# Kernel optimization log

Hardware: AMD Instinct MI355X
Metric: run time of the kernel (lower is better)

Reference implementation:

```python
import jax, jax.numpy as jnp
import numpy as np

H, W, R = 512, 512, 4
H8, W8 = H // 8, W // 8  # 64, 64
B, C = 4, 256


def _offsets(r):
    # diamond window: y in [-r, r], x in [|y|-r, r-|y|]  ->  2r^2+2r+1 offsets
    offs = []
    for y in range(-r, r + 1):
        for x in range(abs(y) - r, r - abs(y) + 1):
            offs.append((y, x))
    return np.asarray(offs, dtype=np.float32)  # [L, 2] = (dy, dx)

_OFFS = _offsets(R)  # L = 41


def _corr_pyramid(f1, f2):
    # over the second image's spatial dims for each pyramid level.
    c = jnp.einsum('bcij,bcuv->bijuv', f1, f2) / jnp.sqrt(jnp.float32(f1.shape[1]))
    pyr = [c]
    for _ in range(3):
        b, i, j, h, w = pyr[-1].shape
        pyr.append(pyr[-1].reshape(b, i, j, h // 2, 2, w // 2, 2).mean(axis=(4, 6)))
    return pyr  # shapes [B,64,64,64/2^k,64/2^k] for k=0..3


def _bilinear_zeros(volf, py, px, h, w):
    # volf: [B,H8,W8,h*w]; py/px: [B,H8,W8,L] pixel coords; zero padding.
    y0 = jnp.floor(py); x0 = jnp.floor(px)
    wy1 = py - y0; wy0 = 1.0 - wy1
    wx1 = px - x0; wx0 = 1.0 - wx1

    def gather(yi, xi):
        valid = (yi >= 0) & (yi < h) & (xi >= 0) & (xi < w)
        yc = jnp.clip(yi, 0, h - 1).astype(jnp.int32)
        xc = jnp.clip(xi, 0, w - 1).astype(jnp.int32)
        v = jnp.take_along_axis(volf, yc * w + xc, axis=-1)
        return jnp.where(valid, v, jnp.zeros((), volf.dtype))

    return (wy0 * wx0 * gather(y0, x0) + wy0 * wx1 * gather(y0, x0 + 1)
            + wy1 * wx0 * gather(y0 + 1, x0) + wy1 * wx1 * gather(y0 + 1, x0 + 1))


def _lookup_level(corr, flow, k):
    # corr: [B,H8,W8,h,w]; flow: [B,2,H8,W8] (chan 0 = dy, chan 1 = dx)
    b, _, _, h, w = corr.shape
    dy = jnp.asarray(_OFFS[:, 0]); dx = jnp.asarray(_OFFS[:, 1])
    ii = jnp.arange(H8, dtype=corr.dtype)[:, None]   # [H8,1]
    jj = jnp.arange(W8, dtype=corr.dtype)[None, :]   # [1,W8]
    scale = jnp.float32(2.0 ** k)
    yc = (ii[None] + flow[:, 0]) / scale             # [B,H8,W8]
    xc = (jj[None] + flow[:, 1]) / scale
    py = yc[..., None] + dy                          # [B,H8,W8,L]
    px = xc[..., None] + dx
    # original normalizes by dim/2 (not (dim-1)/2), grid_sample align_corners=True
    # maps normalized g -> pixel (g+1)*(dim-1)/2, net: pixel = coord*(dim-1)/dim
    py = py * (h - 1) / h
    px = px * (w - 1) / w
    volf = corr.reshape(b, H8, W8, h * w)
    return _bilinear_zeros(volf, py, px, h, w)       # [B,H8,W8,L]


def setup_inputs() -> dict:
    key = jax.random.key(0)
    k1, k2, k3 = jax.random.split(key, 3)
    feat1 = jax.random.normal(k1, (B, C, H8, W8), dtype=jnp.float32)
    feat2 = jax.random.normal(k2, (B, C, H8, W8), dtype=jnp.float32)
    curr_flow = jax.random.normal(k3, (B, 2, H8, W8), dtype=jnp.float32)
    return {"feat1": feat1, "feat2": feat2, "curr_flow": curr_flow}


def reference(feat1, feat2, curr_flow):
    pyr = _corr_pyramid(feat1, feat2)
    lookups = [_lookup_level(pyr[k], curr_flow, k) for k in range(4)]
    return jnp.stack(lookups, axis=3)  # [B, H8, W8, 4, 41]
```

## Files before the change

kernel.cpp:

```cpp
#include <hip/hip_runtime.h>
#include <stdint.h>

#define NB 4
#define NC 256
#define FB   1392640
#define LVO1 1048576
#define LVO2 1310720
#define LVO3 1376256

typedef short bf16x8 __attribute__((ext_vector_type(8)));
typedef float f32x4  __attribute__((ext_vector_type(4)));

__device__ __forceinline__ unsigned short f2b(float x){
  uint32_t u = __float_as_uint(x);
  return (unsigned short)((u + 0x7FFFu + ((u >> 16) & 1u)) >> 16);
}
__device__ __forceinline__ unsigned int pack2(float a, float b){
  return (unsigned int)f2b(a) | ((unsigned int)f2b(b) << 16);
}

__global__ __launch_bounds__(256) void prep_all(const float* __restrict__ f2,
                 unsigned short* __restrict__ f2c){
  __shared__ float lds[128*65];
  __shared__ float l1s[32*65];
  __shared__ float l2s[8*65];
  const int t = threadIdx.x;
  const int fid = blockIdx.x;
  const int b = fid >> 7, rest = fid & 127;
  const int reg = rest >> 2, cc = rest & 3;
  const int i0 = (reg >> 2) * 8, j0 = (reg & 3) * 16;
  const int c0 = cc * 64, qb = cc * 8;

  #pragma unroll
  for (int it = 0; it < 8; ++it){
    int q = t + 256*it;
    int ch = q >> 5, rc = q & 31, ri = rc >> 2, c4 = rc & 3;
    const float4 v = *(const float4*)(f2 + ((size_t)(b*NC) + c0 + ch)*4096
                                        + (i0+ri)*64 + j0 + c4*4);
    float* dstL = lds + (ri*16 + c4*4)*65 + ch;
    dstL[0] = v.x; dstL[65] = v.y; dstL[130] = v.z; dstL[195] = v.w;
  }
  __syncthreads();
  unsigned short* f2cB = f2c + (size_t)b*FB;

  #pragma unroll
  for (int it = 0; it < 4; ++it){
    int idx = t + 256*it;
    int cell = idx & 127, qi = idx >> 7;
    int ci = cell >> 4, cj = cell & 15;
    const float* src = lds + cell*65 + qi*8;
    uint4 v;
    v.x = pack2(src[0], src[1]); v.y = pack2(src[2], src[3]);
    v.z = pack2(src[4], src[5]); v.w = pack2(src[6], src[7]);
    int cellg = (i0+ci)*64 + j0+cj;
    *(uint4*)(f2cB + ((size_t)(qb+qi)*4096 + cellg)*8) = v;
  }
  {
    int cell = t & 31, qi = t >> 5;
    int a = cell >> 3, bc = cell & 7;
    const float* p00 = lds + ((2*a)*16 + 2*bc)*65 + qi*8;
    float s[8];
    #pragma unroll
    for (int j = 0; j < 8; ++j){
      s[j] = p00[j] + p00[65+j] + p00[16*65+j] + p00[17*65+j];
      l1s[cell*65 + qi*8 + j] = s[j];
    }
    uint4 v;
    v.x = pack2(s[0]*0.25f, s[1]*0.25f); v.y = pack2(s[2]*0.25f, s[3]*0.25f);
    v.z = pack2(s[4]*0.25f, s[5]*0.25f); v.w = pack2(s[6]*0.25f, s[7]*0.25f);
    int cellg = ((i0>>1)+a)*32 + (j0>>1)+bc;
    *(uint4*)(f2cB + LVO1 + ((size_t)(qb+qi)*1024 + cellg)*8) = v;
  }
  __syncthreads();
  if (t < 64){
    int cell = t & 7, qi = t >> 3;
    int a2 = cell >> 2, bc2 = cell & 3;
    float s[8];
    #pragma unroll
    for (int j = 0; j < 8; ++j){
      int ch = qi*8 + j;
      s[j] = l1s[((2*a2)*8   + 2*bc2  )*65 + ch] + l1s[((2*a2)*8   + 2*bc2+1)*65 + ch]
           + l1s[((2*a2+1)*8 + 2*bc2  )*65 + ch] + l1s[((2*a2+1)*8 + 2*bc2+1)*65 + ch];
      l2s[cell*65 + ch] = s[j];
    }
    uint4 v;
    v.x = pack2(s[0]*0.0625f, s[1]*0.0625f); v.y = pack2(s[2]*0.0625f, s[3]*0.0625f);
    v.z = pack2(s[4]*0.0625f, s[5]*0.0625f); v.w = pack2(s[6]*0.0625f, s[7]*0.0625f);
    int cellg = ((i0>>2)+a2)*16 + (j0>>2)+bc2;
    *(uint4*)(f2cB + LVO2 + ((size_t)(qb+qi)*256 + cellg)*8) = v;
  }
  __syncthreads();
  if (t < 16){
    int cl = t & 1, qi = t >> 1;
    float s[8];
    #pragma unroll
    for (int j = 0; j < 8; ++j){
      int ch = qi*8 + j;
      s[j] = l2s[(0*4 + 2*cl)*65 + ch] + l2s[(0*4 + 2*cl+1)*65 + ch]
           + l2s[(1*4 + 2*cl)*65 + ch] + l2s[(1*4 + 2*cl+1)*65 + ch];
    }
    const float m = 1.0f/64.0f;
    uint4 v;
    v.x = pack2(s[0]*m, s[1]*m); v.y = pack2(s[2]*m, s[3]*m);
    v.z = pack2(s[4]*m, s[5]*m); v.w = pack2(s[6]*m, s[7]*m);
    int cellg = (i0>>3)*8 + (j0>>3) + cl;
    *(uint4*)(f2cB + LVO3 + ((size_t)(qb+qi)*64 + cellg)*8) = v;
  }
}

__global__ __launch_bounds__(256, 4) void lookup_main(const float* __restrict__ flow,
                 const float* __restrict__ f1,
                 const unsigned short* __restrict__ f2c,
                 float* __restrict__ out){
  const int lane = threadIdx.x & 63;
  const int wid  = threadIdx.x >> 6;
  const int blk = blockIdx.x;
  const int xs = blk & 7;
  const int bb = xs >> 1;
  const int tile = ((blk >> 3) << 1) | (xs & 1);
  const int ti4 = (tile >> 4) << 2;
  const int tj4 = (tile & 15) << 2;

  __shared__ float box[4*16*113];
  __shared__ unsigned short f1s[16*264];
  __shared__ int   ls_y0[64], ls_x0[64];
  __shared__ float ls_f[32];
  __shared__ int   ls_meta[32];

  {
    float4* b4 = (float4*)box;
    for (int q = threadIdx.x; q < (4*16*113)/4; q += 256)
      b4[q] = make_float4(0.f, 0.f, 0.f, 0.f);
  }

  {
    const float* f1b = f1 + ((size_t)(bb*NC) + threadIdx.x)*4096;
    #pragma unroll
    for (int r = 0; r < 4; ++r){
      const float4 v = *(const float4*)(f1b + (ti4 + r)*64 + tj4);
      const int px = r*4;
      f1s[(px+0)*264 + threadIdx.x] = f2b(v.x);
      f1s[(px+1)*264 + threadIdx.x] = f2b(v.y);
      f1s[(px+2)*264 + threadIdx.x] = f2b(v.z);
      f1s[(px+3)*264 + threadIdx.x] = f2b(v.w);
    }
  }

  const int n = lane & 15;
  const int g = lane >> 4;
  const int pn = ((ti4 + (n >> 2)) << 6) + tj4 + (n & 3);

  if (wid == 0){
    const int k = g;
    const int i_n = pn >> 6, j_n = pn & 63;
    const float fy = flow[((bb*2 + 0)*64 + i_n)*64 + j_n];
    const float fx = flow[((bb*2 + 1)*64 + i_n)*64 + j_n];
    if (k == 0){ ls_f[n] = fy; ls_f[16 + n] = fx; }
    const int h = 64 >> k;
    const float inv = 1.0f / (float)(1 << k);
    const float s = (float)(h - 1) / (float)h;
    const float yc = ((float)i_n + fy) * inv;
    const float xc = ((float)j_n + fx) * inv;
    const int y0 = (int)floorf((yc - 4.0f) * s);
    const int x0 = (int)floorf((xc - 4.0f) * s);
    ls_y0[k*16 + n] = y0;
    ls_x0[k*16 + n] = x0;
    int ymin = y0, ymax = y0, xmin = x0, xmax = x0;
    #pragma unroll
    for (int m = 1; m < 16; m <<= 1){
      ymin = min(ymin, __shfl_xor(ymin, m));
      ymax = max(ymax, __shfl_xor(ymax, m));
      xmin = min(xmin, __shfl_xor(xmin, m));
      xmax = max(xmax, __shfl_xor(xmax, m));
    }
    if (n == 0){
      int ylo = max(ymin, 0), yhi = min(ymax + 9, h - 1);
      int xlo = max(xmin, 0), xhi = min(xmax + 9, h - 1);
      int H = max(yhi - ylo + 1, 0), W = max(xhi - xlo + 1, 0);
      int cells = W * H;
      ls_meta[k*8 + 0] = ylo;
      ls_meta[k*8 + 1] = xlo;
      ls_meta[k*8 + 2] = W;
      ls_meta[k*8 + 3] = cells;
      ls_meta[k*8 + 4] = __float_as_int(1.0f / (float)W);
      ls_meta[k*8 + 5] = (k==0) ? 0 : (k==1) ? LVO1 : (k==2) ? LVO2 : LVO3;
      ls_meta[k*8 + 6] = (cells + 15) >> 4;
    }
  }
  __syncthreads();

  bf16x8 bfr[8];
  #pragma unroll
  for (int st = 0; st < 8; ++st)
    bfr[st] = *(const bf16x8*)(&f1s[n*264 + st*32 + g*8]);

  const int y0n0 = ls_y0[n],      x0n0 = ls_x0[n];
  const int y0n1 = ls_y0[16 + n], x0n1 = ls_x0[16 + n];
  const int y0n2 = ls_y0[32 + n], x0n2 = ls_x0[32 + n];
  const int y0n3 = ls_y0[48 + n], x0n3 = ls_x0[48 + n];
  const int pre1 = ls_meta[6];
  const int pre2 = pre1 + ls_meta[14];
  const int pre3 = pre2 + ls_meta[22];
  const int P    = pre3 + ls_meta[30];
  const unsigned short* f2cB = f2c + (size_t)bb*FB;

  for (int p = wid; p < P; p += 4){
    const int k  = (p >= pre1) + (p >= pre2) + (p >= pre3);
    const int lp = p - ((k==0) ? 0 : (k==1) ? pre1 : (k==2) ? pre2 : pre3);
    const int mb = k*8;
    const int ylo = ls_meta[mb], xlo = ls_meta[mb+1], W = ls_meta[mb+2];
    const int cells = ls_meta[mb+3];
    const float rW = __int_as_float(ls_meta[mb+4]);
    const int lvoc = ls_meta[mb+5];
    const int h = 64 >> k;
    const int ncl = h*h;
    const int base = lp << 4;

    const int idxA = min(base + n, cells - 1);
    const int by = (int)fmaf((float)idxA, rW, 0.004f);
    const int bx = idxA - by*W;
    const int cellIdx = (ylo + by)*h + (xlo + bx);
    const unsigned short* colp = f2cB + lvoc + ((size_t)(g*ncl + cellIdx) << 3);
    const int strideS = ncl << 5;

    f32x4 acc0 = {0.f,0.f,0.f,0.f}, acc1 = {0.f,0.f,0.f,0.f};
    #pragma unroll
    for (int st = 0; st < 8; st += 2){
      bf16x8 a0 = *(const bf16x8*)(colp + (size_t)st*strideS);
      bf16x8 a1 = *(const bf16x8*)(colp + (size_t)(st+1)*strideS);
      acc0 = __builtin_amdgcn_mfma_f32_16x16x32_bf16(a0, bfr[st],   acc0, 0, 0, 0);
      acc1 = __builtin_amdgcn_mfma_f32_16x16x32_bf16(a1, bfr[st+1], acc1, 0, 0, 0);
    }
    const int yb = (k==0) ? y0n0 : (k==1) ? y0n1 : (k==2) ? y0n2 : y0n3;
    const int xb = (k==0) ? x0n0 : (k==1) ? x0n1 : (k==2) ? x0n2 : x0n3;
    #pragma unroll
    for (int r = 0; r < 4; ++r){
      const int ci = base + (g << 2) + r;
      if (ci < cells){
        const int byc = (int)fmaf((float)ci, rW, 0.004f);
        const int bxc = ci - byc*W;
        const int ry = ylo + byc - yb;
        const int rx = xlo + bxc - xb;
        if ((unsigned)ry < 10u && (unsigned)rx < 10u)
          box[(k*16 + n)*113 + ry*10 + rx] = (acc0[r] + acc1[r]) * 0.0625f;
      }
    }
  }
  __syncthreads();

  int dy = 0, dx = 0;
  {
    int rem = lane;
    #pragma unroll
    for (int ry = -4; ry <= 4; ++ry){
      int ab = ry < 0 ? -ry : ry;
      int ln = 9 - 2*ab;
      if (rem >= 0 && rem < ln){ dy = ry; dx = rem + (ab - 4); }
      rem -= ln;
    }
  }
  const int k = wid;
  const float inv = 1.0f / (float)(1 << k);
  const float s = (float)((64 >> k) - 1) / (float)(64 >> k);
  if (lane < 41){
    for (int t = 0; t < 16; ++t){
      const int pt = ((ti4 + (t >> 2)) << 6) + tj4 + (t & 3);
      const float fy = ls_f[t], fx = ls_f[16 + t];
      const float yc = ((float)(pt >> 6) + fy) * inv;
      const float xc = ((float)(pt & 63) + fx) * inv;
      const float py = (yc + (float)dy) * s;
      const float px = (xc + (float)dx) * s;
      const float fy0 = floorf(py), fx0 = floorf(px);
      const float wy1 = py - fy0, wx1 = px - fx0;
      const float wy0 = 1.0f - wy1, wx0 = 1.0f - wx1;
      const int iy = (int)fy0 - ls_y0[k*16 + t];
      const int ix = (int)fx0 - ls_x0[k*16 + t];
      const float* bx_ = &box[(k*16 + t)*113 + iy*10 + ix];
      const float v = wy0*(wx0*bx_[0] + wx1*bx_[1]) + wy1*(wx0*bx_[10] + wx1*bx_[11]);
      out[((size_t)(bb*4096 + pt)*4 + k)*41 + lane] = v;
    }
  }
}

extern "C" void kernel_launch(void* const* d_in, const int* in_sizes, int n_in,
                              void* d_out, int out_size, void* d_ws, size_t ws_size,
                              hipStream_t stream){
  const float* feat1 = (const float*)d_in[0];
  const float* feat2 = (const float*)d_in[1];
  const float* flow  = (const float*)d_in[2];
  float* out = (float*)d_out;
  unsigned short* f2c = (unsigned short*)d_ws;

  prep_all<<<512, 256, 0, stream>>>(feat2, f2c);
  lookup_main<<<1024, 256, 0, stream>>>(flow, feat1, f2c, out);
}
```

Baseline: 107.5 us.

## Software-pipeline correlation column loads across lookup passes in lookup_main

Restructures the per-wave pass loop so the eight bf16 column fragments for the next pass are loaded while the current pass's MFMAs run. Pass metadata computation moves into a macro that is evaluated one iteration ahead, and the loop becomes a do-while with a prologue load. The aim is to hide global-load latency behind the matrix ops. In exchange it needs more live VGPRs under a 4-waves-per-SIMD launch bound, and it always issues one speculative extra pass of loads, which rely on the clamped index staying in bounds.

```diff
diff --git a/kernel.cpp b/kernel.cpp
--- a/kernel.cpp
+++ b/kernel.cpp
@@ -107,6 +107,25 @@
     *(uint4*)(f2cB + LVO3 + ((size_t)(qb+qi)*64 + cellg)*8) = v;
   }
 }
+
+#define MKPASS(pp, oK, oBase, oCells, oW, oYlo, oXlo, oYb, oXb, oRW, oColp, oStride) \
+  do { \
+    oK = (pp >= pre1) + (pp >= pre2) + (pp >= pre3); \
+    const int lp_ = pp - ((oK==0) ? 0 : (oK==1) ? pre1 : (oK==2) ? pre2 : pre3); \
+    const int mb_ = oK*8; \
+    oYlo = ls_meta[mb_]; oXlo = ls_meta[mb_+1]; oW = ls_meta[mb_+2]; \
+    oCells = ls_meta[mb_+3]; oRW = __int_as_float(ls_meta[mb_+4]); \
+    const int lvoc_ = ls_meta[mb_+5]; \
+    const int h_ = 64 >> oK, ncl_ = h_*h_; \
+    oBase = lp_ << 4; \
+    const int idxA_ = min(oBase + n, oCells - 1); \
+    const int by_ = (int)fmaf((float)idxA_, oRW, 0.004f); \
+    const int bx_ = idxA_ - by_*oW; \
+    oColp = f2cB + lvoc_ + ((size_t)(g*ncl_ + (oYlo + by_)*h_ + (oXlo + bx_)) << 3); \
+    oStride = ncl_ << 5; \
+    oYb = (oK==0) ? y0n0 : (oK==1) ? y0n1 : (oK==2) ? y0n2 : y0n3; \
+    oXb = (oK==0) ? x0n0 : (oK==1) ? x0n1 : (oK==2) ? x0n2 : x0n3; \
+  } while(0)
 
 __global__ __launch_bounds__(256, 4) void lookup_main(const float* __restrict__ flow,
                  const float* __restrict__ f1,
@@ -204,47 +223,61 @@
   const int P    = pre3 + ls_meta[30];
   const unsigned short* f2cB = f2c + (size_t)bb*FB;
 
-  for (int p = wid; p < P; p += 4){
-    const int k  = (p >= pre1) + (p >= pre2) + (p >= pre3);
-    const int lp = p - ((k==0) ? 0 : (k==1) ? pre1 : (k==2) ? pre2 : pre3);
-    const int mb = k*8;
-    const int ylo = ls_meta[mb], xlo = ls_meta[mb+1], W = ls_meta[mb+2];
-    const int cells = ls_meta[mb+3];
-    const float rW = __int_as_float(ls_meta[mb+4]);
-    const int lvoc = ls_meta[mb+5];
-    const int h = 64 >> k;
-    const int ncl = h*h;
-    const int base = lp << 4;
-
-    const int idxA = min(base + n, cells - 1);
-    const int by = (int)fmaf((float)idxA, rW, 0.004f);
-    const int bx = idxA - by*W;
-    const int cellIdx = (ylo + by)*h + (xlo + bx);
-    const unsigned short* colp = f2cB + lvoc + ((size_t)(g*ncl + cellIdx) << 3);
-    const int strideS = ncl << 5;
-
-    f32x4 acc0 = {0.f,0.f,0.f,0.f}, acc1 = {0.f,0.f,0.f,0.f};
-    #pragma unroll
-    for (int st = 0; st < 8; st += 2){
-      bf16x8 a0 = *(const bf16x8*)(colp + (size_t)st*strideS);
-      bf16x8 a1 = *(const bf16x8*)(colp + (size_t)(st+1)*strideS);
-      acc0 = __builtin_amdgcn_mfma_f32_16x16x32_bf16(a0, bfr[st],   acc0, 0, 0, 0);
-      acc1 = __builtin_amdgcn_mfma_f32_16x16x32_bf16(a1, bfr[st+1], acc1, 0, 0, 0);
-    }
-    const int yb = (k==0) ? y0n0 : (k==1) ? y0n1 : (k==2) ? y0n2 : y0n3;
-    const int xb = (k==0) ? x0n0 : (k==1) ? x0n1 : (k==2) ? x0n2 : x0n3;
-    #pragma unroll
-    for (int r = 0; r < 4; ++r){
-      const int ci = base + (g << 2) + r;
-      if (ci < cells){
-        const int byc = (int)fmaf((float)ci, rW, 0.004f);
-        const int bxc = ci - byc*W;
-        const int ry = ylo + byc - yb;
-        const int rx = xlo + bxc - xb;
-        if ((unsigned)ry < 10u && (unsigned)rx < 10u)
-          box[(k*16 + n)*113 + ry*10 + rx] = (acc0[r] + acc1[r]) * 0.0625f;
+  {
+    int p = wid;
+    int cK, cBase, cCells, cW, cYlo, cXlo, cYb, cXb, cStride;
+    float cRW;
+    const unsigned short* cColp;
+    MKPASS(p, cK, cBase, cCells, cW, cYlo, cXlo, cYb, cXb, cRW, cColp, cStride);
+    bf16x8 af0 = *(const bf16x8*)(cColp);
+    bf16x8 af1 = *(const bf16x8*)(cColp + (size_t)cStride);
+    bf16x8 af2 = *(const bf16x8*)(cColp + (size_t)2*cStride);
+    bf16x8 af3 = *(const bf16x8*)(cColp + (size_t)3*cStride);
+    bf16x8 af4 = *(const bf16x8*)(cColp + (size_t)4*cStride);
+    bf16x8 af5 = *(const bf16x8*)(cColp + (size_t)5*cStride);
+    bf16x8 af6 = *(const bf16x8*)(cColp + (size_t)6*cStride);
+    bf16x8 af7 = *(const bf16x8*)(cColp + (size_t)7*cStride);
+    do {
+      const int np = p + 4;
+      int nK, nBase, nCells, nW, nYlo, nXlo, nYb, nXb, nStride;
+      float nRW;
+      const unsigned short* nColp;
+      MKPASS(np, nK, nBase, nCells, nW, nYlo, nXlo, nYb, nXb, nRW, nColp, nStride);
+
+      f32x4 acc0 = {0.f,0.f,0.f,0.f}, acc1 = {0.f,0.f,0.f,0.f};
+      acc0 = __builtin_amdgcn_mfma_f32_16x16x32_bf16(af0, bfr[0], acc0, 0, 0, 0);
+      acc1 = __builtin_amdgcn_mfma_f32_16x16x32_bf16(af1, bfr[1], acc1, 0, 0, 0);
+      af0 = *(const bf16x8*)(nColp);
+      af1 = *(const bf16x8*)(nColp + (size_t)nStride);
+      acc0 = __builtin_amdgcn_mfma_f32_16x16x32_bf16(af2, bfr[2], acc0, 0, 0, 0);
+      acc1 = __builtin_amdgcn_mfma_f32_16x16x32_bf16(af3, bfr[3], acc1, 0, 0, 0);
+      af2 = *(const bf16x8*)(nColp + (size_t)2*nStride);
+      af3 = *(const bf16x8*)(nColp + (size_t)3*nStride);
+      acc0 = __builtin_amdgcn_mfma_f32_16x16x32_bf16(af4, bfr[4], acc0, 0, 0, 0);
+      acc1 = __builtin_amdgcn_mfma_f32_16x16x32_bf16(af5, bfr[5], acc1, 0, 0, 0);
+      af4 = *(const bf16x8*)(nColp + (size_t)4*nStride);
+      af5 = *(const bf16x8*)(nColp + (size_t)5*nStride);
+      acc0 = __builtin_amdgcn_mfma_f32_16x16x32_bf16(af6, bfr[6], acc0, 0, 0, 0);
+      acc1 = __builtin_amdgcn_mfma_f32_16x16x32_bf16(af7, bfr[7], acc1, 0, 0, 0);
+      af6 = *(const bf16x8*)(nColp + (size_t)6*nStride);
+      af7 = *(const bf16x8*)(nColp + (size_t)7*nStride);
+
+      #pragma unroll
+      for (int r = 0; r < 4; ++r){
+        const int ci = cBase + (g << 2) + r;
+        if (ci < cCells){
+          const int byc = (int)fmaf((float)ci, cRW, 0.004f);
+          const int bxc = ci - byc*cW;
+          const int ry = cYlo + byc - cYb;
+          const int rx = cXlo + bxc - cXb;
+          if ((unsigned)ry < 10u && (unsigned)rx < 10u)
+            box[(cK*16 + n)*113 + ry*10 + rx] = (acc0[r] + acc1[r]) * 0.0625f;
+        }
       }
-    }
+      cK = nK; cBase = nBase; cCells = nCells; cW = nW; cRW = nRW;
+      cYlo = nYlo; cXlo = nXlo; cYb = nYb; cXb = nXb;
+      p = np;
+    } while (p < P);
   }
   __syncthreads();
 
```

Result: no change. 108.2 us (+0.6%).
